# Kernel tuning notes

Hardware: AMD Instinct MI355X
Metric: run time of the kernel (lower is better)

Reference implementation:

```python
import jax, jax.numpy as jnp
import numpy as np

N_NODES = 50000
D = 128
N_EDGES = 800000


def _gcn_layer(h, W, b, row, col, mask, n_nodes):
    # Linear: h @ W.T + b  (nn.Linear convention)
    h = h @ W.T + b
    # degree of source nodes, counting only non-self-loop edges (remove_self_loops)
    deg = jax.ops.segment_sum(mask.astype(h.dtype), row, num_segments=n_nodes)
    deg_inv_sqrt = jnp.where(deg > 0, jax.lax.rsqrt(jnp.maximum(deg, 1.0)), 0.0)
    norm = deg_inv_sqrt[row] * deg_inv_sqrt[col] * mask.astype(h.dtype)
    # gather-scale messages [E, D], scatter-add into target nodes (col)
    msg = norm[:, None] * h[row]
    return jax.ops.segment_sum(msg, col, num_segments=n_nodes)


def setup_inputs() -> dict:
    key = jax.random.key(0)
    ks = jax.random.split(key, 9)
    x = jax.random.normal(ks[0], (N_NODES, D), dtype=jnp.float32)
    edge_index = jax.random.randint(ks[1], (2, N_EDGES), 0, N_NODES, dtype=jnp.int64)
    lim = 1.0 / np.sqrt(D)
    params = {}
    for i in range(3):
        params[f"W{i}"] = jax.random.uniform(ks[2 + 2 * i], (D, D), jnp.float32, -lim, lim)
        params[f"b{i}"] = jax.random.uniform(ks[3 + 2 * i], (D,), jnp.float32, -lim, lim)
    return {"x": x, "edge_index": edge_index, **params}


def reference(x, edge_index, W0, b0, W1, b1, W2, b2):
    row, col = edge_index[0], edge_index[1]
    mask = row != col  # remove_self_loops
    h = x
    for W, b in ((W0, b0), (W1, b1), (W2, b2)):
        h_new = jax.nn.relu(_gcn_layer(h, W, b, row, col, mask, x.shape[0]))
        h = h + h_new
    return h
```

## Files before the change

### kernel.cpp

```cpp
#include <hip/hip_runtime.h>
#include <hip/hip_bf16.h>


#define D_DIM 128
#define SCAN_CHUNK 1024
#define CHUNKS 256
#define GROUPS 8
#define GS (CHUNKS / GROUPS)
#define LDSW 12512

typedef __attribute__((ext_vector_type(8))) short bf16x8;
typedef __attribute__((ext_vector_type(4))) float f32x4;

static __device__ __forceinline__ short f2bf(float f) {
    union { __hip_bfloat16 b; short s; } u;
    u.b = __float2bfloat16(f);
    return u.s;
}
static __device__ __forceinline__ float bf_lo(unsigned p) { return __uint_as_float(p << 16); }
static __device__ __forceinline__ float bf_hi(unsigned p) { return __uint_as_float(p & 0xffff0000u); }


__global__ __launch_bounds__(256) void hist_kernel(const int* __restrict__ ei,
                                                   unsigned* __restrict__ partial_col,
                                                   unsigned* __restrict__ partial_row,
                                                   const float* __restrict__ W0,
                                                   const float* __restrict__ W1,
                                                   const float* __restrict__ W2,
                                                   unsigned short* __restrict__ Wb,
                                                   int E, int CHSZ) {
    int tid = threadIdx.x;
    if (blockIdx.y == 2) {
        int i = blockIdx.x * 256 + tid;
        if (i < 3 * D_DIM * D_DIM) {
            const float* W = (i < 16384) ? W0 : (i < 32768) ? W1 : W2;
            Wb[i] = (unsigned short)f2bf(W[i & 16383]);
        }
        return;
    }
    __shared__ unsigned hh[LDSW];
    int ch = blockIdx.x;
    int docol = (blockIdx.y == 0);
    for (int i = tid; i < LDSW; i += 256) hh[i] = 0u;
    __syncthreads();
    int e0 = ch * CHSZ, e1 = min(e0 + CHSZ, E);
    for (int e = e0 + tid; e < e1; e += 256) {
        int row = ei[e];
        int col = ei[E + e];
        if (row == col) continue;
        int bin = docol ? col : row;
        atomicAdd(&hh[bin >> 2], 1u << ((bin & 3) * 8));
    }
    __syncthreads();
    unsigned* dst = (docol ? partial_col : partial_row) + (size_t)ch * LDSW;
    for (int i = tid; i < LDSW; i += 256) dst[i] = hh[i];
}

__global__ __launch_bounds__(256) void group_prefix_kernel(
    unsigned* __restrict__ partial_col, const unsigned* __restrict__ partial_row,
    unsigned* __restrict__ gsum_col, unsigned* __restrict__ gsum_row, int NW) {
    int w = blockIdx.x * 256 + threadIdx.x;
    if (w >= NW) return;
    int g = blockIdx.y;
    size_t base = (size_t)(g * GS) * LDSW + w;
    if (blockIdx.z == 0) {
        unsigned run = 0;
#pragma unroll 4
        for (int c = 0; c < GS; c++) {
            unsigned v = partial_col[base + (size_t)c * LDSW];
            partial_col[base + (size_t)c * LDSW] = run;
            run += v;
        }
        gsum_col[g * NW + w] = run;
    } else {
        unsigned run = 0;
#pragma unroll 4
        for (int c = 0; c < GS; c++) run += partial_row[base + (size_t)c * LDSW];
        gsum_row[g * NW + w] = run;
    }
}

__global__ __launch_bounds__(256) void cnt_dis_kernel(
    const unsigned* __restrict__ gsum_col, const unsigned* __restrict__ gsum_row,
    int* __restrict__ col_cnt, float* __restrict__ dis, int* __restrict__ bsum, int NW) {
    __shared__ int wsum[4];
    int w = blockIdx.x * 256 + threadIdx.x;
    int s = 0;
    if (w < NW) {
        unsigned clo = 0, chi = 0, rlo = 0, rhi = 0;
#pragma unroll
        for (int g = 0; g < GROUPS; g++) {
            unsigned wc = gsum_col[g * NW + w];
            unsigned wr = gsum_row[g * NW + w];
            clo += wc & 0x00FF00FFu; chi += (wc >> 8) & 0x00FF00FFu;
            rlo += wr & 0x00FF00FFu; rhi += (wr >> 8) & 0x00FF00FFu;
        }
        int c0 = clo & 0xFFFF, c1 = chi & 0xFFFF, c2 = clo >> 16, c3 = chi >> 16;
        int r0 = rlo & 0xFFFF, r1 = rhi & 0xFFFF, r2 = rlo >> 16, r3 = rhi >> 16;
        ((int4*)col_cnt)[w] = make_int4(c0, c1, c2, c3);
        float4 dv;
        dv.x = (r0 > 0) ? rsqrtf((float)r0) : 0.0f;
        dv.y = (r1 > 0) ? rsqrtf((float)r1) : 0.0f;
        dv.z = (r2 > 0) ? rsqrtf((float)r2) : 0.0f;
        dv.w = (r3 > 0) ? rsqrtf((float)r3) : 0.0f;
        ((float4*)dis)[w] = dv;
        s = c0 + c1 + c2 + c3;
    }
#pragma unroll
    for (int d = 32; d > 0; d >>= 1) s += __shfl_down(s, d, 64);
    int lane = threadIdx.x & 63, wv = threadIdx.x >> 6;
    if (lane == 0) wsum[wv] = s;
    __syncthreads();
    if (threadIdx.x == 0) bsum[blockIdx.x] = wsum[0] + wsum[1] + wsum[2] + wsum[3];
}

__global__ __launch_bounds__(256) void scan_final_kernel(const int* __restrict__ cnt,
                                                         const int* __restrict__ bsum,
                                                         int* __restrict__ offs,
                                                         int n, int G) {
    __shared__ int wsum[4];
    __shared__ int sblock;
    int base = blockIdx.x * SCAN_CHUNK;
    int tid = threadIdx.x;
    const int PT = SCAN_CHUNK / 256;
    int v[PT];
    int s = 0;
#pragma unroll
    for (int i = 0; i < PT; i++) {
        int g = base + tid * PT + i;
        v[i] = (g < n) ? cnt[g] : 0;
        s += v[i];
    }
    int local_sum = s;
    int lane = tid & 63, w = tid >> 6;
#pragma unroll
    for (int d = 1; d < 64; d <<= 1) {
        int t = __shfl_up(s, d, 64);
        if (lane >= d) s += t;
    }
    if (lane == 63) wsum[w] = s;
    if (tid < 64) {
        int bv = (tid < G) ? bsum[tid] : 0;
        int bs = bv;
#pragma unroll
        for (int d = 1; d < 64; d <<= 1) {
            int t = __shfl_up(bs, d, 64);
            if (tid >= d) bs += t;
        }
        if (tid == blockIdx.x) sblock = bs - bv;
        if (tid == 63 && blockIdx.x == G - 1) offs[n] = bs;
    }
    __syncthreads();
    int wbase = 0;
    for (int i = 0; i < w; i++) wbase += wsum[i];
    int run = sblock + wbase + (s - local_sum);
#pragma unroll
    for (int i = 0; i < PT; i++) {
        int g = base + tid * PT + i;
        if (g < n) offs[g] = run;
        run += v[i];
    }
}

__global__ __launch_bounds__(256) void scatter_kernel(const int* __restrict__ ei,
                                                      const float* __restrict__ dis,
                                                      const int* __restrict__ offs,
                                                      const unsigned* __restrict__ chpref,
                                                      const unsigned* __restrict__ gsum_col,
                                                      unsigned* __restrict__ epack,
                                                      int E, int CHSZ, int NW) {
    __shared__ unsigned cur[LDSW];
    int tid = threadIdx.x;
    int ch = blockIdx.x;
    int g = ch / GS;
    const unsigned* pf = chpref + (size_t)ch * LDSW;
    for (int i = tid; i < LDSW; i += 256) {
        unsigned seed = pf[i];
        if (i < NW)
            for (int gp = 0; gp < g; gp++) seed += gsum_col[gp * NW + i];
        cur[i] = seed;
    }
    __syncthreads();
    int e0 = ch * CHSZ, e1 = min(e0 + CHSZ, E);
    for (int e = e0 + tid; e < e1; e += 256) {
        int row = ei[e];
        int col = ei[E + e];
        if (row == col) continue;
        float wgt = dis[row] * dis[col];
        int wd = col >> 2, sh = (col & 3) * 8;
        unsigned old = atomicAdd(&cur[wd], 1u << sh);
        int slot = offs[col] + (int)((old >> sh) & 0xFFu);
        epack[slot] = (unsigned)row | ((unsigned)(unsigned short)f2bf(wgt) << 16);
    }
}


__global__ __launch_bounds__(256) void linear_mfma_kernel(
    const float* __restrict__ A, const unsigned short* __restrict__ Wb,
    const float* __restrict__ bias, unsigned short* __restrict__ hWb, int nrows) {
    __shared__ unsigned short stage[4][16 * 136];
    int wave = threadIdx.x >> 6;
    int lane = threadIdx.x & 63;
    int r0 = blockIdx.x * 64 + wave * 16;
    int m = lane & 15, q = lane >> 4;
    int rload = min(r0 + m, nrows - 1);
    const float4* h4 = (const float4*)A;

    f32x4 acc[8];
#pragma unroll
    for (int jt = 0; jt < 8; jt++) acc[jt] = (f32x4){0.f, 0.f, 0.f, 0.f};

#pragma unroll
    for (int k0 = 0; k0 < 128; k0 += 32) {
        int c0 = k0 + q * 8;
        float4 x0 = h4[rload * 32 + (c0 >> 2)];
        float4 x1 = h4[rload * 32 + (c0 >> 2) + 1];
        bf16x8 a;
        a[0] = f2bf(x0.x); a[1] = f2bf(x0.y); a[2] = f2bf(x0.z); a[3] = f2bf(x0.w);
        a[4] = f2bf(x1.x); a[5] = f2bf(x1.y); a[6] = f2bf(x1.z); a[7] = f2bf(x1.w);
#pragma unroll
        for (int jt = 0; jt < 8; jt++) {
            bf16x8 b = *(const bf16x8*)(Wb + (jt * 16 + m) * D_DIM + c0);
            acc[jt] = __builtin_amdgcn_mfma_f32_16x16x32_bf16(a, b, acc[jt], 0, 0, 0);
        }
    }

#pragma unroll
    for (int jt = 0; jt < 8; jt++) {
        float bv = bias[jt * 16 + m];
#pragma unroll
        for (int reg = 0; reg < 4; reg++)
            stage[wave][(q * 4 + reg) * 136 + jt * 16 + m] =
                (unsigned short)f2bf(acc[jt][reg] + bv);
    }
#pragma unroll
    for (int t = 0; t < 4; t++) {
        int rl = t * 4 + (lane >> 4);
        int gr = r0 + rl;
        if (gr < nrows) {
            uint4 v = *(const uint4*)&stage[wave][rl * 136 + (lane & 15) * 8];
            *(uint4*)&hWb[(size_t)gr * D_DIM + (lane & 15) * 8] = v;
        }
    }
}

__global__ __launch_bounds__(256) void agg_kernel(const int* __restrict__ offs,
                                                  const unsigned* __restrict__ epack,
                                                  const unsigned int* __restrict__ hW2,
                                                  const float* __restrict__ hprev,
                                                  float* __restrict__ hout, int n_nodes) {
    int node = (int)((blockIdx.x * blockDim.x + threadIdx.x) >> 6);
    int lane = threadIdx.x & 63;
    if (node >= n_nodes) return;

    int beg = offs[node];
    int end = offs[node + 1];

    float ax8[8], ay8[8];
#pragma unroll
    for (int u = 0; u < 8; u++) { ax8[u] = 0.f; ay8[u] = 0.f; }

    int i = beg;
    for (; i + 8 <= end; i += 8) {
        unsigned e[8];
        unsigned p[8];
#pragma unroll
        for (int u = 0; u < 8; u++) e[u] = epack[i + u];
#pragma unroll
        for (int u = 0; u < 8; u++) p[u] = hW2[((e[u] & 0xffffu) << 6) + lane];
#pragma unroll
        for (int u = 0; u < 8; u++) {
            float w = bf_hi(e[u]);
            ax8[u] = fmaf(w, bf_lo(p[u]), ax8[u]);
            ay8[u] = fmaf(w, bf_hi(p[u]), ay8[u]);
        }
    }
    int rem = end - i;
    if (rem & 4) {
        unsigned e[4];
        unsigned p[4];
#pragma unroll
        for (int u = 0; u < 4; u++) e[u] = epack[i + u];
#pragma unroll
        for (int u = 0; u < 4; u++) p[u] = hW2[((e[u] & 0xffffu) << 6) + lane];
#pragma unroll
        for (int u = 0; u < 4; u++) {
            float w = bf_hi(e[u]);
            ax8[u] = fmaf(w, bf_lo(p[u]), ax8[u]);
            ay8[u] = fmaf(w, bf_hi(p[u]), ay8[u]);
        }
        i += 4;
    }
    if (rem & 2) {
        unsigned e0 = epack[i], e1 = epack[i + 1];
        unsigned p0 = hW2[((e0 & 0xffffu) << 6) + lane];
        unsigned p1 = hW2[((e1 & 0xffffu) << 6) + lane];
        float w0 = bf_hi(e0), w1 = bf_hi(e1);
        ax8[4] = fmaf(w0, bf_lo(p0), ax8[4]); ay8[4] = fmaf(w0, bf_hi(p0), ay8[4]);
        ax8[5] = fmaf(w1, bf_lo(p1), ax8[5]); ay8[5] = fmaf(w1, bf_hi(p1), ay8[5]);
        i += 2;
    }
    if (rem & 1) {
        unsigned e0 = epack[i];
        unsigned p0 = hW2[((e0 & 0xffffu) << 6) + lane];
        float w0 = bf_hi(e0);
        ax8[6] = fmaf(w0, bf_lo(p0), ax8[6]); ay8[6] = fmaf(w0, bf_hi(p0), ay8[6]);
    }
    float ax = ((ax8[0] + ax8[1]) + (ax8[2] + ax8[3])) + ((ax8[4] + ax8[5]) + (ax8[6] + ax8[7]));
    float ay = ((ay8[0] + ay8[1]) + (ay8[2] + ay8[3])) + ((ay8[4] + ay8[5]) + (ay8[6] + ay8[7]));

    int idx = node * (D_DIM / 2) + lane;
    float2 hv = ((const float2*)hprev)[idx];
    float2 o;
    o.x = hv.x + fmaxf(ax, 0.0f);
    o.y = hv.y + fmaxf(ay, 0.0f);
    ((float2*)hout)[idx] = o;
}


static inline size_t align_up(size_t x, size_t a) { return (x + a - 1) & ~(a - 1); }

extern "C" void kernel_launch(void* const* d_in, const int* in_sizes, int n_in,
                              void* d_out, int out_size, void* d_ws, size_t ws_size,
                              hipStream_t stream) {
    const float* x = (const float*)d_in[0];
    const int* ei = (const int*)d_in[1];
    const float* Wl[3] = {(const float*)d_in[2], (const float*)d_in[4], (const float*)d_in[6]};
    const float* bl[3] = {(const float*)d_in[3], (const float*)d_in[5], (const float*)d_in[7]};

    const int N = in_sizes[0] / D_DIM;
    const int E = in_sizes[1] / 2;
    const int NW = N / 4;
    const int G = (N + SCAN_CHUNK - 1) / SCAN_CHUNK;
    const int NWB = (NW + 255) / 256;
    const int CHSZ = (E + CHUNKS - 1) / CHUNKS;

    char* p = (char*)d_ws;
    int* col_cnt = (int*)p;            p += align_up((size_t)N * 4, 256);
    int* offs    = (int*)p;            p += align_up((size_t)(N + 1) * 4, 256);
    float* dis   = (float*)p;          p += align_up((size_t)N * 4, 256);
    int* bsum    = (int*)p;            p += align_up((size_t)64 * 4, 256);
    unsigned* partial_col = (unsigned*)p;  p += align_up((size_t)CHUNKS * LDSW * 4, 256);
    unsigned* partial_row = (unsigned*)p;  p += align_up((size_t)CHUNKS * LDSW * 4, 256);
    unsigned* gsum_col = (unsigned*)p; p += align_up((size_t)GROUPS * NW * 4, 256);
    unsigned* gsum_row = (unsigned*)p; p += align_up((size_t)GROUPS * NW * 4, 256);
    unsigned short* Wb = (unsigned short*)p;  p += align_up((size_t)3 * D_DIM * D_DIM * 2, 256);
    unsigned* epack = (unsigned*)p;    p += align_up((size_t)E * 4, 256);
    unsigned short* hWb = (unsigned short*)p;  p += align_up((size_t)N * D_DIM * 2, 256);
    (void)ws_size;

    hist_kernel<<<dim3(CHUNKS, 3), 256, 0, stream>>>(ei, partial_col, partial_row,
                                                     Wl[0], Wl[1], Wl[2], Wb, E, CHSZ);
    group_prefix_kernel<<<dim3(NWB, GROUPS, 2), 256, 0, stream>>>(partial_col, partial_row,
                                                                  gsum_col, gsum_row, NW);
    cnt_dis_kernel<<<NWB, 256, 0, stream>>>(gsum_col, gsum_row, col_cnt, dis, bsum, NW);
    scan_final_kernel<<<G, 256, 0, stream>>>(col_cnt, bsum, offs, N, G);
    scatter_kernel<<<CHUNKS, 256, 0, stream>>>(ei, dis, offs, partial_col, gsum_col,
                                               epack, E, CHSZ, NW);

    const float* hprev = x;
    float* h = (float*)d_out;
    int gemm_blocks = (N + 63) / 64;
    int agg_blocks = (N + 3) / 4;
    for (int l = 0; l < 3; l++) {
        linear_mfma_kernel<<<gemm_blocks, 256, 0, stream>>>(hprev, Wb + l * 16384, bl[l], hWb, N);
        agg_kernel<<<agg_blocks, 256, 0, stream>>>(offs, epack, (const unsigned int*)hWb, hprev, h, N);
        hprev = h;
    }
}
```

Measured before the change: 341.2 us.

## Vectorize aggregation gathers to 16-byte loads across edge quarter-waves

The aggregation kernel now splits each 64-lane wave into four 16-lane groups. Each group processes a different edge and loads a full 256-byte bf16 row with uint4 loads, so every lane fetches 16 bytes per edge where it used to fetch 4. The partial sums are then reduced across groups with cross-lane shuffles, and a single group writes the output using float4 stores. Separately, cnt_dis now writes exclusive prefixes of the per-group column counts, so the scatter seed needs one load instead of a loop over previous groups. The costs are the extra shuffle reduction, idle lanes on the final output write, and partly wasted lanes on the remainder edges.

```diff
diff --git a/kernel.cpp b/kernel.cpp
--- a/kernel.cpp
+++ b/kernel.cpp
@@ -81,19 +81,27 @@
 }
 
 __global__ __launch_bounds__(256) void cnt_dis_kernel(
-    const unsigned* __restrict__ gsum_col, const unsigned* __restrict__ gsum_row,
+    unsigned* __restrict__ gsum_col, const unsigned* __restrict__ gsum_row,
     int* __restrict__ col_cnt, float* __restrict__ dis, int* __restrict__ bsum, int NW) {
     __shared__ int wsum[4];
     int w = blockIdx.x * 256 + threadIdx.x;
     int s = 0;
     if (w < NW) {
+        unsigned wcv[GROUPS];
         unsigned clo = 0, chi = 0, rlo = 0, rhi = 0;
 #pragma unroll
         for (int g = 0; g < GROUPS; g++) {
             unsigned wc = gsum_col[g * NW + w];
             unsigned wr = gsum_row[g * NW + w];
+            wcv[g] = wc;
             clo += wc & 0x00FF00FFu; chi += (wc >> 8) & 0x00FF00FFu;
             rlo += wr & 0x00FF00FFu; rhi += (wr >> 8) & 0x00FF00FFu;
+        }
+        unsigned run = 0;
+#pragma unroll
+        for (int g = 0; g < GROUPS; g++) {
+            gsum_col[g * NW + w] = run;
+            run += wcv[g];
         }
         int c0 = clo & 0xFFFF, c1 = chi & 0xFFFF, c2 = clo >> 16, c3 = chi >> 16;
         int r0 = rlo & 0xFFFF, r1 = rhi & 0xFFFF, r2 = rlo >> 16, r3 = rhi >> 16;
@@ -166,18 +174,17 @@
                                                       const float* __restrict__ dis,
                                                       const int* __restrict__ offs,
                                                       const unsigned* __restrict__ chpref,
-                                                      const unsigned* __restrict__ gsum_col,
+                                                      const unsigned* __restrict__ gpref,
                                                       unsigned* __restrict__ epack,
                                                       int E, int CHSZ, int NW) {
     __shared__ unsigned cur[LDSW];
     int tid = threadIdx.x;
     int ch = blockIdx.x;
-    int g = ch / GS;
     const unsigned* pf = chpref + (size_t)ch * LDSW;
+    const unsigned* gb = gpref + (size_t)(ch / GS) * NW;
     for (int i = tid; i < LDSW; i += 256) {
         unsigned seed = pf[i];
-        if (i < NW)
-            for (int gp = 0; gp < g; gp++) seed += gsum_col[gp * NW + i];
+        if (i < NW) seed += gb[i];
         cur[i] = seed;
     }
     __syncthreads();
@@ -246,75 +253,75 @@
 
 __global__ __launch_bounds__(256) void agg_kernel(const int* __restrict__ offs,
                                                   const unsigned* __restrict__ epack,
-                                                  const unsigned int* __restrict__ hW2,
+                                                  const uint4* __restrict__ hW4,
                                                   const float* __restrict__ hprev,
                                                   float* __restrict__ hout, int n_nodes) {
     int node = (int)((blockIdx.x * blockDim.x + threadIdx.x) >> 6);
     int lane = threadIdx.x & 63;
     if (node >= n_nodes) return;
+    int g = lane >> 4, s = lane & 15;
 
     int beg = offs[node];
     int end = offs[node + 1];
 
-    float ax8[8], ay8[8];
-#pragma unroll
-    for (int u = 0; u < 8; u++) { ax8[u] = 0.f; ay8[u] = 0.f; }
+    float acc[8];
+#pragma unroll
+    for (int k = 0; k < 8; k++) acc[k] = 0.f;
 
     int i = beg;
     for (; i + 8 <= end; i += 8) {
-        unsigned e[8];
-        unsigned p[8];
-#pragma unroll
-        for (int u = 0; u < 8; u++) e[u] = epack[i + u];
-#pragma unroll
-        for (int u = 0; u < 8; u++) p[u] = hW2[((e[u] & 0xffffu) << 6) + lane];
-#pragma unroll
-        for (int u = 0; u < 8; u++) {
-            float w = bf_hi(e[u]);
-            ax8[u] = fmaf(w, bf_lo(p[u]), ax8[u]);
-            ay8[u] = fmaf(w, bf_hi(p[u]), ay8[u]);
-        }
-    }
-    int rem = end - i;
-    if (rem & 4) {
-        unsigned e[4];
-        unsigned p[4];
-#pragma unroll
-        for (int u = 0; u < 4; u++) e[u] = epack[i + u];
-#pragma unroll
-        for (int u = 0; u < 4; u++) p[u] = hW2[((e[u] & 0xffffu) << 6) + lane];
-#pragma unroll
-        for (int u = 0; u < 4; u++) {
-            float w = bf_hi(e[u]);
-            ax8[u] = fmaf(w, bf_lo(p[u]), ax8[u]);
-            ay8[u] = fmaf(w, bf_hi(p[u]), ay8[u]);
-        }
-        i += 4;
-    }
-    if (rem & 2) {
-        unsigned e0 = epack[i], e1 = epack[i + 1];
-        unsigned p0 = hW2[((e0 & 0xffffu) << 6) + lane];
-        unsigned p1 = hW2[((e1 & 0xffffu) << 6) + lane];
+        unsigned e0 = epack[i + g];
+        unsigned e1 = epack[i + 4 + g];
+        uint4 p0 = hW4[(e0 & 0xffffu) * 16 + s];
+        uint4 p1 = hW4[(e1 & 0xffffu) * 16 + s];
         float w0 = bf_hi(e0), w1 = bf_hi(e1);
-        ax8[4] = fmaf(w0, bf_lo(p0), ax8[4]); ay8[4] = fmaf(w0, bf_hi(p0), ay8[4]);
-        ax8[5] = fmaf(w1, bf_lo(p1), ax8[5]); ay8[5] = fmaf(w1, bf_hi(p1), ay8[5]);
-        i += 2;
-    }
-    if (rem & 1) {
-        unsigned e0 = epack[i];
-        unsigned p0 = hW2[((e0 & 0xffffu) << 6) + lane];
-        float w0 = bf_hi(e0);
-        ax8[6] = fmaf(w0, bf_lo(p0), ax8[6]); ay8[6] = fmaf(w0, bf_hi(p0), ay8[6]);
-    }
-    float ax = ((ax8[0] + ax8[1]) + (ax8[2] + ax8[3])) + ((ax8[4] + ax8[5]) + (ax8[6] + ax8[7]));
-    float ay = ((ay8[0] + ay8[1]) + (ay8[2] + ay8[3])) + ((ay8[4] + ay8[5]) + (ay8[6] + ay8[7]));
-
-    int idx = node * (D_DIM / 2) + lane;
-    float2 hv = ((const float2*)hprev)[idx];
-    float2 o;
-    o.x = hv.x + fmaxf(ax, 0.0f);
-    o.y = hv.y + fmaxf(ay, 0.0f);
-    ((float2*)hout)[idx] = o;
+        acc[0] = fmaf(w0, bf_lo(p0.x), acc[0]); acc[1] = fmaf(w0, bf_hi(p0.x), acc[1]);
+        acc[2] = fmaf(w0, bf_lo(p0.y), acc[2]); acc[3] = fmaf(w0, bf_hi(p0.y), acc[3]);
+        acc[4] = fmaf(w0, bf_lo(p0.z), acc[4]); acc[5] = fmaf(w0, bf_hi(p0.z), acc[5]);
+        acc[6] = fmaf(w0, bf_lo(p0.w), acc[6]); acc[7] = fmaf(w0, bf_hi(p0.w), acc[7]);
+        acc[0] = fmaf(w1, bf_lo(p1.x), acc[0]); acc[1] = fmaf(w1, bf_hi(p1.x), acc[1]);
+        acc[2] = fmaf(w1, bf_lo(p1.y), acc[2]); acc[3] = fmaf(w1, bf_hi(p1.y), acc[3]);
+        acc[4] = fmaf(w1, bf_lo(p1.z), acc[4]); acc[5] = fmaf(w1, bf_hi(p1.z), acc[5]);
+        acc[6] = fmaf(w1, bf_lo(p1.w), acc[6]); acc[7] = fmaf(w1, bf_hi(p1.w), acc[7]);
+    }
+    if (i < end) {
+        unsigned e0 = epack[min(i + g, end - 1)];
+        float w0 = (i + g < end) ? bf_hi(e0) : 0.f;
+        uint4 p0 = hW4[(e0 & 0xffffu) * 16 + s];
+        acc[0] = fmaf(w0, bf_lo(p0.x), acc[0]); acc[1] = fmaf(w0, bf_hi(p0.x), acc[1]);
+        acc[2] = fmaf(w0, bf_lo(p0.y), acc[2]); acc[3] = fmaf(w0, bf_hi(p0.y), acc[3]);
+        acc[4] = fmaf(w0, bf_lo(p0.z), acc[4]); acc[5] = fmaf(w0, bf_hi(p0.z), acc[5]);
+        acc[6] = fmaf(w0, bf_lo(p0.w), acc[6]); acc[7] = fmaf(w0, bf_hi(p0.w), acc[7]);
+        if (i + 4 < end) {
+            unsigned e1 = epack[min(i + 4 + g, end - 1)];
+            float w1 = (i + 4 + g < end) ? bf_hi(e1) : 0.f;
+            uint4 p1 = hW4[(e1 & 0xffffu) * 16 + s];
+            acc[0] = fmaf(w1, bf_lo(p1.x), acc[0]); acc[1] = fmaf(w1, bf_hi(p1.x), acc[1]);
+            acc[2] = fmaf(w1, bf_lo(p1.y), acc[2]); acc[3] = fmaf(w1, bf_hi(p1.y), acc[3]);
+            acc[4] = fmaf(w1, bf_lo(p1.z), acc[4]); acc[5] = fmaf(w1, bf_hi(p1.z), acc[5]);
+            acc[6] = fmaf(w1, bf_lo(p1.w), acc[6]); acc[7] = fmaf(w1, bf_hi(p1.w), acc[7]);
+        }
+    }
+
+#pragma unroll
+    for (int k = 0; k < 8; k++) {
+        acc[k] += __shfl_xor(acc[k], 16, 64);
+        acc[k] += __shfl_xor(acc[k], 32, 64);
+    }
+
+    if (g == 0) {
+        const float4* hp4 = (const float4*)hprev;
+        float4* ho4 = (float4*)hout;
+        int idx = node * 32 + s * 2;
+        float4 h0 = hp4[idx], h1 = hp4[idx + 1];
+        float4 o0, o1;
+        o0.x = h0.x + fmaxf(acc[0], 0.f); o0.y = h0.y + fmaxf(acc[1], 0.f);
+        o0.z = h0.z + fmaxf(acc[2], 0.f); o0.w = h0.w + fmaxf(acc[3], 0.f);
+        o1.x = h1.x + fmaxf(acc[4], 0.f); o1.y = h1.y + fmaxf(acc[5], 0.f);
+        o1.z = h1.z + fmaxf(acc[6], 0.f); o1.w = h1.w + fmaxf(acc[7], 0.f);
+        ho4[idx] = o0;
+        ho4[idx + 1] = o1;
+    }
 }
 
 
@@ -364,7 +371,7 @@
     int agg_blocks = (N + 3) / 4;
     for (int l = 0; l < 3; l++) {
         linear_mfma_kernel<<<gemm_blocks, 256, 0, stream>>>(hprev, Wb + l * 16384, bl[l], hWb, N);
-        agg_kernel<<<agg_blocks, 256, 0, stream>>>(offs, epack, (const unsigned int*)hWb, hprev, h, N);
+        agg_kernel<<<agg_blocks, 256, 0, stream>>>(offs, epack, (const uint4*)hWb, hprev, h, N);
         hprev = h;
     }
 }
```

Result: faster. 311.7 us (-8.6%).
